# Kernel tuning notes

Measured on AMD Instinct MI355X. Metric: run time of the kernel, lower is better.

Reference implementation:

```python
import jax, jax.numpy as jnp
import numpy as np


def setup_inputs() -> dict:
    key = jax.random.key(0)
    k1, k2 = jax.random.split(key)
    B, T, D = 32, 1024, 384
    encodings = jax.random.normal(k1, (B, T, D), dtype=jnp.float32)
    durations = jax.random.randint(k2, (B, T), 0, 8, dtype=jnp.int32)
    return {"encodings": encodings, "durations": durations}


def reference(encodings, durations):
    # encodings: [B, T, D] float; durations: [B, T] int (torch code rounds .item())
    B, T, D = encodings.shape
    reps = jnp.round(durations).astype(jnp.int32)            # [B, T]
    csum = jnp.cumsum(reps, axis=1)                          # [B, T] exclusive end offsets
    totals = csum[:, -1]                                     # [B] expanded length per batch
    # max_len computed from concrete durations (dynamic output length, like the torch code)
    max_len = int(jnp.max(totals))
    pos = jnp.arange(max_len)                                # [L]
    # frame p belongs to token j where csum[j-1] <= p < csum[j] -> searchsorted right
    idx = jax.vmap(lambda c: jnp.searchsorted(c, pos, side="right"))(csum)  # [B, L]
    idx = jnp.minimum(idx, T - 1)
    out = jnp.take_along_axis(encodings, idx[:, :, None], axis=1)           # [B, L, D]
    mask = pos[None, :] < totals[:, None]                                   # [B, L]
    return jnp.where(mask[:, :, None], out, jnp.zeros((), dtype=encodings.dtype))
```

## Files before the change

kernel.cpp:

```cpp
#include <hip/hip_runtime.h>

#define NB 32
#define NT 1024
#define ND 384
#define ND4 (ND / 4)
#define THREADS 256
#define ILP 8
#define CHUNK (THREADS * ILP)

typedef float vfloat4 __attribute__((ext_vector_type(4)));

__global__ void __launch_bounds__(NT)
scan_scatter_kernel(const int* __restrict__ dur,
                    int* __restrict__ idx,
                    int* __restrict__ totals,
                    int max_len) {
    __shared__ int wsum[16];
    const int b = blockIdx.x;
    const int t = threadIdx.x;
    const int lane = t & 63;
    const int w = t >> 6;
    const int d = dur[b * NT + t];

    int x = d;
    #pragma unroll
    for (int off = 1; off < 64; off <<= 1) {
        int y = __shfl_up(x, off, 64);
        if (lane >= off) x += y;
    }
    if (lane == 63) wsum[w] = x;
    __syncthreads();
    if (w == 0) {
        int v = (lane < 16) ? wsum[lane] : 0;
        #pragma unroll
        for (int off = 1; off < 16; off <<= 1) {
            int y = __shfl_up(v, off, 64);
            if (lane >= off) v += y;
        }
        if (lane < 16) wsum[lane] = v;
    }
    __syncthreads();
    const int csum_t = x + (w ? wsum[w - 1] : 0);
    const int total  = wsum[15];

    int* idx_b = idx + (size_t)b * max_len;
    for (int p = csum_t - d; p < csum_t; ++p)
        idx_b[p] = t;
    for (int p = total + t; p < max_len; p += NT)
        idx_b[p] = 0;
    if (t == NT - 1)
        totals[b] = total;
}

__global__ void __launch_bounds__(THREADS)
gather_kernel(const vfloat4* __restrict__ enc,
              const int* __restrict__ idx,
              const int* __restrict__ totals,
              vfloat4* __restrict__ out,
              int max_len, int f4_per_batch) {
    const int b = blockIdx.y;
    const int total_f4 = totals[b] * ND4;
    const int* idx_b = idx + (size_t)b * max_len;
    const vfloat4* enc_b = enc + (size_t)b * NT * ND4;
    vfloat4* out_b = out + (size_t)b * (size_t)max_len * ND4;

    const int base = blockIdx.x * CHUNK + threadIdx.x;

    int j[ILP], t[ILP], d4[ILP];
    #pragma unroll
    for (int k = 0; k < ILP; ++k) {
        j[k] = base + k * THREADS;
        const int jc = j[k] < f4_per_batch ? j[k] : f4_per_batch - 1;
        const int p  = jc / ND4;
        d4[k] = jc - p * ND4;
        t[k]  = idx_b[p];
    }
    vfloat4 v[ILP];
    #pragma unroll
    for (int k = 0; k < ILP; ++k)
        v[k] = enc_b[(size_t)t[k] * ND4 + d4[k]];
    #pragma unroll
    for (int k = 0; k < ILP; ++k) {
        if (j[k] >= total_f4)
            v[k] = (vfloat4){0.f, 0.f, 0.f, 0.f};
        if (j[k] < f4_per_batch)
            __builtin_nontemporal_store(v[k], &out_b[j[k]]);
    }
}

extern "C" void kernel_launch(void* const* d_in, const int* in_sizes, int n_in,
                              void* d_out, int out_size, void* d_ws, size_t ws_size,
                              hipStream_t stream) {
    const float* enc = (const float*)d_in[0];
    const int*   dur = (const int*)d_in[1];
    float* out = (float*)d_out;

    const int max_len = out_size / (NB * ND);

    int* totals = (int*)d_ws;
    int* idx    = totals + NB;

    scan_scatter_kernel<<<NB, NT, 0, stream>>>(dur, idx, totals, max_len);

    const int f4pb = max_len * ND4;
    const int blocks_x = (f4pb + CHUNK - 1) / CHUNK;
    dim3 grid(blocks_x, NB);
    gather_kernel<<<grid, THREADS, 0, stream>>>(
        (const vfloat4*)enc, idx, totals, (vfloat4*)out, max_len, f4pb);
}
```

Baseline: 220.9 us.

## Fuse scan into gather kernel with per-block binary search over shared prefix sums

Removes the separate scan/scatter kernel and the global index buffer. Each gather block recomputes the batch's prefix sum of durations in shared memory and binary-searches the source token for the roughly 22 frames its chunk covers. This drops one launch, the serialized single-block-per-batch scatter, and the global idx round trip. The cost is that every block redundantly loads and scans 1024 durations and adds two extra barriers.

```diff
diff --git a/kernel.cpp b/kernel.cpp
--- a/kernel.cpp
+++ b/kernel.cpp
@@ -7,78 +7,82 @@
 #define THREADS 256
 #define ILP 8
 #define CHUNK (THREADS * ILP)
+#define MAXF 24
 
 typedef float vfloat4 __attribute__((ext_vector_type(4)));
 
-__global__ void __launch_bounds__(NT)
-scan_scatter_kernel(const int* __restrict__ dur,
-                    int* __restrict__ idx,
-                    int* __restrict__ totals,
-                    int max_len) {
-    __shared__ int wsum[16];
-    const int b = blockIdx.x;
-    const int t = threadIdx.x;
-    const int lane = t & 63;
-    const int w = t >> 6;
-    const int d = dur[b * NT + t];
+__global__ void __launch_bounds__(THREADS)
+fused_kernel(const vfloat4* __restrict__ enc,
+             const int* __restrict__ dur,
+             vfloat4* __restrict__ out,
+             int max_len, int f4_per_batch) {
+    __shared__ int s_csum[NT];
+    __shared__ int s_wsum[4];
+    __shared__ int s_t[MAXF];
 
-    int x = d;
+    const int b    = blockIdx.y;
+    const int tid  = threadIdx.x;
+    const int lane = tid & 63;
+    const int w    = tid >> 6;
+
+    const int4 dv = ((const int4*)(dur + b * NT))[tid];
+    const int l0 = dv.x;
+    const int l1 = l0 + dv.y;
+    const int l2 = l1 + dv.z;
+    const int l3 = l2 + dv.w;
+    int x = l3;
     #pragma unroll
     for (int off = 1; off < 64; off <<= 1) {
         int y = __shfl_up(x, off, 64);
         if (lane >= off) x += y;
     }
-    if (lane == 63) wsum[w] = x;
+    if (lane == 63) s_wsum[w] = x;
     __syncthreads();
-    if (w == 0) {
-        int v = (lane < 16) ? wsum[lane] : 0;
-        #pragma unroll
-        for (int off = 1; off < 16; off <<= 1) {
-            int y = __shfl_up(v, off, 64);
-            if (lane >= off) v += y;
+    int base = x - l3;
+    #pragma unroll
+    for (int i = 0; i < 3; ++i)
+        if (w > i) base += s_wsum[i];
+    s_csum[4 * tid + 0] = base + l0;
+    s_csum[4 * tid + 1] = base + l1;
+    s_csum[4 * tid + 2] = base + l2;
+    s_csum[4 * tid + 3] = base + l3;
+    __syncthreads();
+    const int total = s_csum[NT - 1];
+
+    const int jbase = blockIdx.x * CHUNK;
+    const int p0    = jbase / ND4;
+    if (tid < MAXF) {
+        const int p = p0 + tid;
+        int res = 0;
+        if (p < total) {
+            int lo = 0, hi = NT - 1;
+            while (lo < hi) {
+                const int mid = (lo + hi) >> 1;
+                if (s_csum[mid] <= p) lo = mid + 1; else hi = mid;
+            }
+            res = lo;
         }
-        if (lane < 16) wsum[lane] = v;
+        s_t[tid] = res;
     }
     __syncthreads();
-    const int csum_t = x + (w ? wsum[w - 1] : 0);
-    const int total  = wsum[15];
 
-    int* idx_b = idx + (size_t)b * max_len;
-    for (int p = csum_t - d; p < csum_t; ++p)
-        idx_b[p] = t;
-    for (int p = total + t; p < max_len; p += NT)
-        idx_b[p] = 0;
-    if (t == NT - 1)
-        totals[b] = total;
-}
-
-__global__ void __launch_bounds__(THREADS)
-gather_kernel(const vfloat4* __restrict__ enc,
-              const int* __restrict__ idx,
-              const int* __restrict__ totals,
-              vfloat4* __restrict__ out,
-              int max_len, int f4_per_batch) {
-    const int b = blockIdx.y;
-    const int total_f4 = totals[b] * ND4;
-    const int* idx_b = idx + (size_t)b * max_len;
+    const int total_f4 = total * ND4;
     const vfloat4* enc_b = enc + (size_t)b * NT * ND4;
     vfloat4* out_b = out + (size_t)b * (size_t)max_len * ND4;
 
-    const int base = blockIdx.x * CHUNK + threadIdx.x;
-
-    int j[ILP], t[ILP], d4[ILP];
+    int j[ILP], tt[ILP], dd[ILP];
     #pragma unroll
     for (int k = 0; k < ILP; ++k) {
-        j[k] = base + k * THREADS;
+        j[k] = jbase + tid + k * THREADS;
         const int jc = j[k] < f4_per_batch ? j[k] : f4_per_batch - 1;
         const int p  = jc / ND4;
-        d4[k] = jc - p * ND4;
-        t[k]  = idx_b[p];
+        dd[k] = jc - p * ND4;
+        tt[k] = s_t[p - p0];
     }
     vfloat4 v[ILP];
     #pragma unroll
     for (int k = 0; k < ILP; ++k)
-        v[k] = enc_b[(size_t)t[k] * ND4 + d4[k]];
+        v[k] = enc_b[(size_t)tt[k] * ND4 + dd[k]];
     #pragma unroll
     for (int k = 0; k < ILP; ++k) {
         if (j[k] >= total_f4)
@@ -96,15 +100,9 @@
     float* out = (float*)d_out;
 
     const int max_len = out_size / (NB * ND);
-
-    int* totals = (int*)d_ws;
-    int* idx    = totals + NB;
-
-    scan_scatter_kernel<<<NB, NT, 0, stream>>>(dur, idx, totals, max_len);
-
     const int f4pb = max_len * ND4;
     const int blocks_x = (f4pb + CHUNK - 1) / CHUNK;
     dim3 grid(blocks_x, NB);
-    gather_kernel<<<grid, THREADS, 0, stream>>>(
-        (const vfloat4*)enc, idx, totals, (vfloat4*)out, max_len, f4pb);
+    fused_kernel<<<grid, THREADS, 0, stream>>>(
+        (const vfloat4*)enc, dur, (vfloat4*)out, max_len, f4pb);
 }
```

Measured after the change: 222.2 us. Within noise of the previous version (+0.6%).
